# Kernel optimization log

Hardware: AMD Instinct MI355X
Metric: run time of the kernel (lower is better)

Reference implementation:

```python
import jax, jax.numpy as jnp
import numpy as np

NQ = 4   # qubits
QL = 2   # strongly-entangling layers
Z_DIAG = jnp.array([1.0, -1.0], jnp.float32)


def _apply_1q_batched(state, U, w):
    # state: [B,2,2,2,2], U: [B,2,2] per-sample gate on wire w
    st = jnp.moveaxis(state, 1 + w, -1)
    st = jnp.einsum('b...i,bji->b...j', st, U)
    return jnp.moveaxis(st, -1, 1 + w)


def _apply_1q_shared(state, U, w):
    # U: [2,2] shared gate on wire w
    st = jnp.moveaxis(state, 1 + w, -1)
    st = jnp.einsum('b...i,ji->b...j', st, U)
    return jnp.moveaxis(st, -1, 1 + w)


def _cnot(state, c, t):
    c_ax, t_ax = 1 + c, 1 + t
    s0 = jax.lax.index_in_dim(state, 0, c_ax, keepdims=True)
    s1 = jax.lax.index_in_dim(state, 1, c_ax, keepdims=True)
    s1 = jnp.flip(s1, axis=t_ax)  # X on target where control==1
    return jnp.concatenate([s0, s1], axis=c_ax)


def _rot_matrix(phi, th, om):
    # PennyLane Rot = RZ(om) RY(th) RZ(phi)
    ct, st = jnp.cos(th * 0.5), jnp.sin(th * 0.5)
    return jnp.stack([
        jnp.stack([jnp.exp(-0.5j * (phi + om)) * ct, -jnp.exp(0.5j * (phi - om)) * st]),
        jnp.stack([jnp.exp(-0.5j * (phi - om)) * st, jnp.exp(0.5j * (phi + om)) * ct]),
    ])


def _quantum(angles, qw):
    # angles: [B,4] RX embedding angles; qw: [QL,NQ,3]
    B = angles.shape[0]
    state = jnp.zeros((B,) + (2,) * NQ, jnp.complex64)
    state = state.at[(slice(None),) + (0,) * NQ].set(1.0)
    # AngleEmbedding: RX(angle_w) on wire w (per-sample gates)
    half = angles.astype(jnp.float32) * 0.5
    c, s = jnp.cos(half), jnp.sin(half)
    for w in range(NQ):
        U = jnp.stack([
            jnp.stack([c[:, w] + 0j, -1j * s[:, w]], -1),
            jnp.stack([-1j * s[:, w], c[:, w] + 0j], -1),
        ], -2)  # [B,2,2]
        state = _apply_1q_batched(state, U, w)
    # StronglyEntanglingLayers: Rot on each wire, then CNOT ring with range r
    qwc = qw.astype(jnp.complex64).real  # keep real, cast inside rot
    for l in range(QL):
        for w in range(NQ):
            U = _rot_matrix(qw[l, w, 0], qw[l, w, 1], qw[l, w, 2])
            state = _apply_1q_shared(state, U, w)
        r = l % (NQ - 1) + 1  # default ranges: [1, 2]
        for w in range(NQ):
            state = _cnot(state, w, (w + r) % NQ)
    probs = state.real ** 2 + state.imag ** 2  # [B,2,2,2,2]
    evs = []
    for w in range(NQ):
        other = tuple(a for a in range(1, NQ + 1) if a != 1 + w)
        evs.append(probs.sum(axis=other) @ Z_DIAG)  # <Z_w>
    return jnp.stack(evs, -1)  # [B,NQ]


def _lstm_last(x, W_ih, W_hh, b_ih, b_hh):
    # torch gate order: i, f, g, o; returns last hidden state [B,H]
    B = x.shape[0]
    H = W_hh.shape[1]
    xz = jnp.einsum('btf,gf->btg', x, W_ih) + b_ih + b_hh  # [B,T,4H]
    def step(carry, z_t):
        h, c = carry
        z = z_t + h @ W_hh.T
        i, f, g, o = jnp.split(z, 4, axis=-1)
        i, f, o = jax.nn.sigmoid(i), jax.nn.sigmoid(f), jax.nn.sigmoid(o)
        g = jnp.tanh(g)
        c = f * c + i * g
        h = o * jnp.tanh(c)
        return (h, c), None
    h0 = jnp.zeros((B, H), x.dtype)
    (h, _), _ = jax.lax.scan(step, (h0, h0), jnp.swapaxes(xz, 0, 1))
    return h


def setup_inputs() -> dict:
    key = jax.random.key(0)
    ks = jax.random.split(key, 10)
    B, T, IN, H = 4096, 256, 1, 50
    sc_ih = 1.0 / np.sqrt(H)
    return {
        'x': jax.random.normal(ks[0], (B, T, IN), jnp.float32),
        'W_ih': jax.random.normal(ks[1], (4 * H, IN), jnp.float32) * sc_ih,
        'W_hh': jax.random.normal(ks[2], (4 * H, H), jnp.float32) * sc_ih,
        'b_ih': jax.random.normal(ks[3], (4 * H,), jnp.float32) * sc_ih,
        'b_hh': jax.random.normal(ks[4], (4 * H,), jnp.float32) * sc_ih,
        'Wp': jax.random.normal(ks[5], (NQ, H), jnp.float32) * sc_ih,
        'bp': jax.random.normal(ks[6], (NQ,), jnp.float32) * sc_ih,
        'qw': jax.random.uniform(ks[7], (QL, NQ, 3), jnp.float32, 0.0, 2.0 * np.pi),
        'Wo': jax.random.normal(ks[8], (1, NQ), jnp.float32) * 0.5,
        'bo': jax.random.normal(ks[9], (1,), jnp.float32) * 0.5,
    }


def reference(x, W_ih, W_hh, b_ih, b_hh, Wp, bp, qw, Wo, bo):
    h = _lstm_last(x, W_ih, W_hh, b_ih, b_hh)          # [B,H]
    angles = jnp.tanh(h @ Wp.T + bp) * (np.pi / 2)     # [B,NQ]
    evs = _quantum(angles, qw)                          # [B,NQ]
    return evs @ Wo.T + bo                              # [B,1]
```

## Files before the change

### kernel.cpp

```cpp
#include <hip/hip_runtime.h>

#define HID 50
#define TSTEPS 256
#define SPB 16
#define NW 7
#define THREADS (NW * 64)
#define XSTRIDE 260

#if __has_builtin(__builtin_amdgcn_exp2f)
#define EXP2(x) __builtin_amdgcn_exp2f(x)
#else
#define EXP2(x) exp2f(x)
#endif
#define L2E 1.44269504088896340736f

typedef __attribute__((ext_vector_type(8))) _Float16 half8;
typedef __attribute__((ext_vector_type(4))) float f32x4;

static __device__ __forceinline__ f32x4 MF16(half8 a, half8 b, f32x4 c) {
    return __builtin_amdgcn_mfma_f32_16x16x32_f16(a, b, c, 0, 0, 0);
}
static __device__ __forceinline__ float sig2(float a) {
    return __builtin_amdgcn_rcpf(1.0f + EXP2(a));
}
static __device__ __forceinline__ float fast_tanh(float x) {
    return 1.0f - 2.0f * sig2(2.0f * L2E * x);
}

static __device__ __forceinline__ int slot_of_unit(int u) {
    return 8 * (u >> 3) + 2 * (u & 3) + ((u >> 2) & 1);
}

__global__ __launch_bounds__(THREADS, 2) void hybrid_lstm_2t(
    const float* __restrict__ x,
    const float* __restrict__ W_ih,
    const float* __restrict__ W_hh,
    const float* __restrict__ b_ih,
    const float* __restrict__ b_hh,
    const float* __restrict__ Wp,
    const float* __restrict__ bp,
    const float* __restrict__ qw,
    const float* __restrict__ Wo,
    const float* __restrict__ bo,
    float* __restrict__ out)
{
    __shared__ __align__(16) float x_lds[SPB * XSTRIDE];
    __shared__ __align__(16) _Float16 h_tab[2][1024];

    const int tid  = threadIdx.x;
    const int wid  = tid >> 6;
    const int lane = tid & 63;
    const int qs   = lane & 15;
    const int g2   = lane >> 4;

    {
        unsigned* hz = (unsigned*)&h_tab[0][0];
        for (int i = tid; i < 1024; i += THREADS) hz[i] = 0u;
        const float* xg = x + (size_t)blockIdx.x * SPB * TSTEPS;
        for (int i = tid; i < SPB * TSTEPS; i += THREADS)
            x_lds[(i >> 8) * XSTRIDE + (i & 255)] = xg[i];
    }

    half8 Ah[2][2];
    {
        const int q    = qs & 3;
        const float sc = (q == 2) ? 2.0f * L2E : -L2E;
#pragma unroll
        for (int ti = 0; ti < 2; ++ti) {
            const int uA  = 8 * wid + 4 * ti + (qs >> 2);
            const bool vr = (uA < HID);
            const int orow = q * HID + (vr ? uA : 0);
#pragma unroll
            for (int kh = 0; kh < 2; ++kh) {
#pragma unroll
                for (int r = 0; r < 8; ++r) {
                    const int s  = kh * 32 + g2 * 8 + r;
                    const int un = 8 * (s >> 3) + 4 * (s & 1) + ((s >> 1) & 3);
                    float v = 0.0f;
                    if (vr && un < HID) v = sc * W_hh[orow * HID + un];
                    Ah[ti][kh][r] = (_Float16)v;
                }
            }
        }
    }

    float wihc[2][4], bsumc[2][4];
    bool cv[2];
    _Float16* wp0[2];
#pragma unroll
    for (int ti = 0; ti < 2; ++ti) {
        const int uC = 8 * wid + 4 * ti + g2;
        cv[ti] = (uC < HID);
#pragma unroll
        for (int reg = 0; reg < 4; ++reg) {
            const float sc = (reg == 2) ? 2.0f * L2E : -L2E;
            const int orow = reg * HID + (cv[ti] ? uC : 0);
            wihc[ti][reg]  = sc * W_ih[orow];
            bsumc[ti][reg] = sc * (b_ih[orow] + b_hh[orow]);
        }
        const int s_w = slot_of_unit(cv[ti] ? uC : 0);
        const int p_w = s_w & 31;
        wp0[ti] = &h_tab[0][(s_w >> 5) * 512 + ((p_w >> 3) * 16 + qs) * 8 + (p_w & 7)];
    }

    __syncthreads();

    float cst0 = 0.0f, cst1 = 0.0f;
    half8 bh0, bh1;
    auto loadB = [&](int buf) {
        const _Float16* bp_ = &h_tab[buf][0] + lane * 8;
        bh0 = *(const half8*)(bp_);
        bh1 = *(const half8*)(bp_ + 512);
    };

    loadB(1);

    const float* xrow = &x_lds[qs * XSTRIDE];

#pragma unroll 1
    for (int t4 = 0; t4 < TSTEPS; t4 += 4) {
        const float4 xq = *(const float4*)(xrow + t4);
#pragma unroll
        for (int k = 0; k < 4; ++k) {
            const float xt = (k == 0) ? xq.x : (k == 1) ? xq.y : (k == 2) ? xq.z : xq.w;
            f32x4 acc0, acc1;
#pragma unroll
            for (int reg = 0; reg < 4; ++reg) {
                acc0[reg] = fmaf(wihc[0][reg], xt, bsumc[0][reg]);
                acc1[reg] = fmaf(wihc[1][reg], xt, bsumc[1][reg]);
            }
            acc0 = MF16(Ah[0][0], bh0, acc0);
            acc1 = MF16(Ah[1][0], bh0, acc1);
            acc0 = MF16(Ah[0][1], bh1, acc0);
            acc1 = MF16(Ah[1][1], bh1, acc1);

            const float i0 = sig2(acc0[0]);
            const float f0 = sig2(acc0[1]);
            const float g0 = 1.0f - 2.0f * sig2(acc0[2]);
            const float o0 = sig2(acc0[3]);
            cst0 = fmaf(f0, cst0, i0 * g0);
            const float h0 = o0 * fast_tanh(cst0);
            const float i1 = sig2(acc1[0]);
            const float f1 = sig2(acc1[1]);
            const float g1 = 1.0f - 2.0f * sig2(acc1[2]);
            const float o1 = sig2(acc1[3]);
            cst1 = fmaf(f1, cst1, i1 * g1);
            const float h1 = o1 * fast_tanh(cst1);

            const int boff = (k & 1) * 1024;
            if (cv[0]) wp0[0][boff] = (_Float16)h0;
            if (cv[1]) wp0[1][boff] = (_Float16)h1;
            __syncthreads();
            loadB(k & 1);
        }
    }

    if (wid < 4) {
        const int sm  = 4 * wid + (lane >> 4);
        const int ql  = lane & 15;
        const int grp = lane & 48;

        const _Float16* t1 = &h_tab[1][0];
        float ang0 = bp[0], ang1 = bp[1], ang2 = bp[2], ang3 = bp[3];
#pragma unroll
        for (int kk = 0; kk < HID; ++kk) {
            const int s   = slot_of_unit(kk);
            const int p   = s & 31;
            const int idx = (s >> 5) * 512 + ((p >> 3) * 16 + sm) * 8 + (p & 7);
            const float hk = (float)t1[idx];
            ang0 = fmaf(Wp[0 * HID + kk], hk, ang0);
            ang1 = fmaf(Wp[1 * HID + kk], hk, ang1);
            ang2 = fmaf(Wp[2 * HID + kk], hk, ang2);
            ang3 = fmaf(Wp[3 * HID + kk], hk, ang3);
        }
        float ang[4];
        ang[0] = fast_tanh(ang0) * 1.57079632679489662f;
        ang[1] = fast_tanh(ang1) * 1.57079632679489662f;
        ang[2] = fast_tanh(ang2) * 1.57079632679489662f;
        ang[3] = fast_tanh(ang3) * 1.57079632679489662f;

        float ar = (ql == 0) ? 1.0f : 0.0f;
        float ai = 0.0f;

#pragma unroll
        for (int wq = 0; wq < 4; ++wq) {
            const int mask = 8 >> wq;
            float s_, c_;
            __sincosf(0.5f * ang[wq], &s_, &c_);
            const float pr = __shfl_xor(ar, mask);
            const float pi = __shfl_xor(ai, mask);
            const float nr = c_ * ar + s_ * pi;
            const float ni = c_ * ai - s_ * pr;
            ar = nr; ai = ni;
        }
#pragma unroll
        for (int l = 0; l < 2; ++l) {
#pragma unroll
            for (int wq = 0; wq < 4; ++wq) {
                const float phi = qw[(l * 4 + wq) * 3 + 0];
                const float th  = qw[(l * 4 + wq) * 3 + 1];
                const float om  = qw[(l * 4 + wq) * 3 + 2];
                float st_, ct_, sa, ca, sb, cb;
                __sincosf(0.5f * th, &st_, &ct_);
                __sincosf(0.5f * (phi + om), &sa, &ca);
                __sincosf(0.5f * (phi - om), &sb, &cb);
                const int mask = 8 >> wq;
                const bool bit = (ql & mask) != 0;
                const float dr  = ca * ct_;
                const float di  = (bit ? sa : -sa) * ct_;
                const float orr = (bit ? cb : -cb) * st_;
                const float oi  = -sb * st_;
                const float pr = __shfl_xor(ar, mask);
                const float pi = __shfl_xor(ai, mask);
                const float nr = dr * ar - di * ai + orr * pr - oi * pi;
                const float ni = dr * ai + di * ar + orr * pi + oi * pr;
                ar = nr; ai = ni;
            }
            const int r = (l % 3) + 1;
#pragma unroll
            for (int wq = 0; wq < 4; ++wq) {
                const int mc  = 8 >> wq;
                const int mt  = 8 >> ((wq + r) % 4);
                const int src = (ql & mc) ? (ql ^ mt) : ql;
                ar = __shfl(ar, grp | src);
                ai = __shfl(ai, grp | src);
            }
        }
        const float prob = ar * ar + ai * ai;
        float coeff = 0.0f;
#pragma unroll
        for (int wq = 0; wq < 4; ++wq) {
            const float sgn = (ql & (8 >> wq)) ? -1.0f : 1.0f;
            coeff = fmaf(sgn, Wo[wq], coeff);
        }
        float v = prob * coeff;
        v += __shfl_xor(v, 1);
        v += __shfl_xor(v, 2);
        v += __shfl_xor(v, 4);
        v += __shfl_xor(v, 8);
        if (ql == 0) out[blockIdx.x * SPB + sm] = v + bo[0];
    }
}

extern "C" void kernel_launch(void* const* d_in, const int* in_sizes, int n_in,
                              void* d_out, int out_size, void* d_ws, size_t ws_size,
                              hipStream_t stream) {
    const float* x    = (const float*)d_in[0];
    const float* W_ih = (const float*)d_in[1];
    const float* W_hh = (const float*)d_in[2];
    const float* b_ih = (const float*)d_in[3];
    const float* b_hh = (const float*)d_in[4];
    const float* Wp   = (const float*)d_in[5];
    const float* bp   = (const float*)d_in[6];
    const float* qw   = (const float*)d_in[7];
    const float* Wo   = (const float*)d_in[8];
    const float* bo   = (const float*)d_in[9];
    float* out = (float*)d_out;

    const int B = in_sizes[0] / TSTEPS;
    hybrid_lstm_2t<<<B / SPB, THREADS, 0, stream>>>(x, W_ih, W_hh, b_ih, b_hh,
                                                    Wp, bp, qw, Wo, bo, out);
}
```

Baseline: 111.4 us.

## Halve samples per block and give each wave four gate tiles

Each block now handles 8 samples with 4 waves instead of 16 samples with 7 waves. Each wave issues four MFMA gate tiles per step, and lanes 8-15 take their results from a cross-lane shuffle, so the padded batch columns are reused for additional hidden units. The h table becomes a plain row-major layout with a padded row stride, which removes the swizzled slot mapping. This doubles the grid and cuts per-block barrier participants, which should improve occupancy and latency hiding on the serial recurrence. The cost is extra shuffles and more MFMA work per wave.

```diff
diff --git a/kernel.cpp b/kernel.cpp
--- a/kernel.cpp
+++ b/kernel.cpp
@@ -2,9 +2,10 @@
 
 #define HID 50
 #define TSTEPS 256
-#define SPB 16
-#define NW 7
+#define SPB 8
+#define NW 4
 #define THREADS (NW * 64)
+#define HROW 72
 #define XSTRIDE 260
 
 #if __has_builtin(__builtin_amdgcn_exp2f)
@@ -27,11 +28,7 @@
     return 1.0f - 2.0f * sig2(2.0f * L2E * x);
 }
 
-static __device__ __forceinline__ int slot_of_unit(int u) {
-    return 8 * (u >> 3) + 2 * (u & 3) + ((u >> 2) & 1);
-}
-
-__global__ __launch_bounds__(THREADS, 2) void hybrid_lstm_2t(
+__global__ __launch_bounds__(THREADS, 2) void hybrid_lstm_4t(
     const float* __restrict__ x,
     const float* __restrict__ W_ih,
     const float* __restrict__ W_hh,
@@ -45,7 +42,7 @@
     float* __restrict__ out)
 {
     __shared__ __align__(16) float x_lds[SPB * XSTRIDE];
-    __shared__ __align__(16) _Float16 h_tab[2][1024];
+    __shared__ __align__(16) _Float16 h_tab[2][16 * HROW];
 
     const int tid  = threadIdx.x;
     const int wid  = tid >> 6;
@@ -55,67 +52,68 @@
 
     {
         unsigned* hz = (unsigned*)&h_tab[0][0];
-        for (int i = tid; i < 1024; i += THREADS) hz[i] = 0u;
+        for (int i = tid; i < 2 * 16 * HROW / 2; i += THREADS) hz[i] = 0u;
         const float* xg = x + (size_t)blockIdx.x * SPB * TSTEPS;
         for (int i = tid; i < SPB * TSTEPS; i += THREADS)
             x_lds[(i >> 8) * XSTRIDE + (i & 255)] = xg[i];
     }
 
-    half8 Ah[2][2];
+    half8 Ah[4][2];
     {
         const int q    = qs & 3;
         const float sc = (q == 2) ? 2.0f * L2E : -L2E;
 #pragma unroll
-        for (int ti = 0; ti < 2; ++ti) {
-            const int uA  = 8 * wid + 4 * ti + (qs >> 2);
+        for (int ti = 0; ti < 4; ++ti) {
+            const int uA  = 4 * (4 * wid + ti) + (qs >> 2);
             const bool vr = (uA < HID);
             const int orow = q * HID + (vr ? uA : 0);
 #pragma unroll
             for (int kh = 0; kh < 2; ++kh) {
 #pragma unroll
                 for (int r = 0; r < 8; ++r) {
-                    const int s  = kh * 32 + g2 * 8 + r;
-                    const int un = 8 * (s >> 3) + 4 * (s & 1) + ((s >> 1) & 3);
+                    const int s = kh * 32 + g2 * 8 + r;
                     float v = 0.0f;
-                    if (vr && un < HID) v = sc * W_hh[orow * HID + un];
+                    if (vr && s < HID) v = sc * W_hh[orow * HID + s];
                     Ah[ti][kh][r] = (_Float16)v;
                 }
             }
         }
     }
 
-    float wihc[2][4], bsumc[2][4];
-    bool cv[2];
-    _Float16* wp0[2];
-#pragma unroll
-    for (int ti = 0; ti < 2; ++ti) {
-        const int uC = 8 * wid + 4 * ti + g2;
-        cv[ti] = (uC < HID);
+    float wihc[4][4], bsumc[4][4];
+#pragma unroll
+    for (int ti = 0; ti < 4; ++ti) {
+        const int uC  = 4 * (4 * wid + ti) + g2;
+        const bool cv = (uC < HID);
 #pragma unroll
         for (int reg = 0; reg < 4; ++reg) {
             const float sc = (reg == 2) ? 2.0f * L2E : -L2E;
-            const int orow = reg * HID + (cv[ti] ? uC : 0);
-            wihc[ti][reg]  = sc * W_ih[orow];
-            bsumc[ti][reg] = sc * (b_ih[orow] + b_hh[orow]);
-        }
-        const int s_w = slot_of_unit(cv[ti] ? uC : 0);
-        const int p_w = s_w & 31;
-        wp0[ti] = &h_tab[0][(s_w >> 5) * 512 + ((p_w >> 3) * 16 + qs) * 8 + (p_w & 7)];
-    }
+            const int orow = reg * HID + (cv ? uC : 0);
+            wihc[ti][reg]  = cv ? sc * W_ih[orow] : 0.0f;
+            bsumc[ti][reg] = cv ? sc * (b_ih[orow] + b_hh[orow]) : 0.0f;
+        }
+    }
+
+    const int s_l  = qs & 7;
+    const bool hi8 = (qs >= 8);
+    const int u0w  = 16 * wid + (hi8 ? 8 : 0) + g2;
+    const int u1w  = u0w + 4;
+    _Float16* const wpA = &h_tab[0][s_l * HROW + u0w];
+    _Float16* const wpB = &h_tab[0][s_l * HROW + u1w];
 
     __syncthreads();
 
-    float cst0 = 0.0f, cst1 = 0.0f;
+    float cstA = 0.0f, cstB = 0.0f;
     half8 bh0, bh1;
     auto loadB = [&](int buf) {
-        const _Float16* bp_ = &h_tab[buf][0] + lane * 8;
+        const _Float16* bp_ = &h_tab[buf][qs * HROW + g2 * 8];
         bh0 = *(const half8*)(bp_);
-        bh1 = *(const half8*)(bp_ + 512);
+        bh1 = *(const half8*)(bp_ + 32);
     };
 
     loadB(1);
 
-    const float* xrow = &x_lds[qs * XSTRIDE];
+    const float* xrow = &x_lds[s_l * XSTRIDE];
 
 #pragma unroll 1
     for (int t4 = 0; t4 < TSTEPS; t4 += 4) {
@@ -123,39 +121,54 @@
 #pragma unroll
         for (int k = 0; k < 4; ++k) {
             const float xt = (k == 0) ? xq.x : (k == 1) ? xq.y : (k == 2) ? xq.z : xq.w;
-            f32x4 acc0, acc1;
+            f32x4 a0, a1, a2, a3;
 #pragma unroll
             for (int reg = 0; reg < 4; ++reg) {
-                acc0[reg] = fmaf(wihc[0][reg], xt, bsumc[0][reg]);
-                acc1[reg] = fmaf(wihc[1][reg], xt, bsumc[1][reg]);
-            }
-            acc0 = MF16(Ah[0][0], bh0, acc0);
-            acc1 = MF16(Ah[1][0], bh0, acc1);
-            acc0 = MF16(Ah[0][1], bh1, acc0);
-            acc1 = MF16(Ah[1][1], bh1, acc1);
-
-            const float i0 = sig2(acc0[0]);
-            const float f0 = sig2(acc0[1]);
-            const float g0 = 1.0f - 2.0f * sig2(acc0[2]);
-            const float o0 = sig2(acc0[3]);
-            cst0 = fmaf(f0, cst0, i0 * g0);
-            const float h0 = o0 * fast_tanh(cst0);
-            const float i1 = sig2(acc1[0]);
-            const float f1 = sig2(acc1[1]);
-            const float g1 = 1.0f - 2.0f * sig2(acc1[2]);
-            const float o1 = sig2(acc1[3]);
-            cst1 = fmaf(f1, cst1, i1 * g1);
-            const float h1 = o1 * fast_tanh(cst1);
-
-            const int boff = (k & 1) * 1024;
-            if (cv[0]) wp0[0][boff] = (_Float16)h0;
-            if (cv[1]) wp0[1][boff] = (_Float16)h1;
+                a0[reg] = fmaf(wihc[0][reg], xt, bsumc[0][reg]);
+                a1[reg] = fmaf(wihc[1][reg], xt, bsumc[1][reg]);
+                a2[reg] = fmaf(wihc[2][reg], xt, bsumc[2][reg]);
+                a3[reg] = fmaf(wihc[3][reg], xt, bsumc[3][reg]);
+            }
+            a0 = MF16(Ah[0][0], bh0, a0);
+            a1 = MF16(Ah[1][0], bh0, a1);
+            a2 = MF16(Ah[2][0], bh0, a2);
+            a3 = MF16(Ah[3][0], bh0, a3);
+            a0 = MF16(Ah[0][1], bh1, a0);
+            a1 = MF16(Ah[1][1], bh1, a1);
+            a2 = MF16(Ah[2][1], bh1, a2);
+            a3 = MF16(Ah[3][1], bh1, a3);
+
+            f32x4 cA, cB;
+#pragma unroll
+            for (int reg = 0; reg < 4; ++reg) {
+                const float r2 = __shfl_xor(a2[reg], 8);
+                const float r3 = __shfl_xor(a3[reg], 8);
+                cA[reg] = hi8 ? r2 : a0[reg];
+                cB[reg] = hi8 ? r3 : a1[reg];
+            }
+
+            const float iA = sig2(cA[0]);
+            const float fA = sig2(cA[1]);
+            const float gA = 1.0f - 2.0f * sig2(cA[2]);
+            const float oA = sig2(cA[3]);
+            cstA = fmaf(fA, cstA, iA * gA);
+            const float hA = oA * fast_tanh(cstA);
+            const float iB = sig2(cB[0]);
+            const float fB = sig2(cB[1]);
+            const float gB = 1.0f - 2.0f * sig2(cB[2]);
+            const float oB = sig2(cB[3]);
+            cstB = fmaf(fB, cstB, iB * gB);
+            const float hB = oB * fast_tanh(cstB);
+
+            const int boff = (k & 1) * (16 * HROW);
+            wpA[boff] = (_Float16)hA;
+            wpB[boff] = (_Float16)hB;
             __syncthreads();
             loadB(k & 1);
         }
     }
 
-    if (wid < 4) {
+    if (wid < 2) {
         const int sm  = 4 * wid + (lane >> 4);
         const int ql  = lane & 15;
         const int grp = lane & 48;
@@ -164,10 +177,7 @@
         float ang0 = bp[0], ang1 = bp[1], ang2 = bp[2], ang3 = bp[3];
 #pragma unroll
         for (int kk = 0; kk < HID; ++kk) {
-            const int s   = slot_of_unit(kk);
-            const int p   = s & 31;
-            const int idx = (s >> 5) * 512 + ((p >> 3) * 16 + sm) * 8 + (p & 7);
-            const float hk = (float)t1[idx];
+            const float hk = (float)t1[sm * HROW + kk];
             ang0 = fmaf(Wp[0 * HID + kk], hk, ang0);
             ang1 = fmaf(Wp[1 * HID + kk], hk, ang1);
             ang2 = fmaf(Wp[2 * HID + kk], hk, ang2);
@@ -258,6 +268,6 @@
     float* out = (float*)d_out;
 
     const int B = in_sizes[0] / TSTEPS;
-    hybrid_lstm_2t<<<B / SPB, THREADS, 0, stream>>>(x, W_ih, W_hh, b_ih, b_hh,
+    hybrid_lstm_4t<<<B / SPB, THREADS, 0, stream>>>(x, W_ih, W_hh, b_ih, b_hh,
                                                     Wp, bp, qw, Wo, bo, out);
 }
```

Result: slower. 159.7 us (+43.3%).
